# Kernel optimization log

Measured on AMD Instinct MI355X. Metric: run time of the kernel, lower is better.

Reference implementation:

```python
import jax, jax.numpy as jnp
import numpy as np

B, S, E = 2, 2048, 2048
H, KV, HD = 16, 4, 128  # num_heads, num_kv_heads, head_dim
G = H // KV             # query heads per kv head
ROPE_BASE = 10000.0


def rope_tables(dim, maxlen):
    freqs = 1.0 / ROPE_BASE ** (jnp.arange(0, dim, 2, dtype=jnp.float32) / dim)
    t = jnp.arange(maxlen, dtype=jnp.float32)
    f = jnp.outer(t, freqs)  # (maxlen, dim//2)
    return jnp.cos(f), jnp.sin(f)


def apply_rope(x, cos, sin):
    # x: (..., seq, heads, head_dim); interleaved-pair rotation
    s_len = x.shape[-3]
    c = cos[:s_len][:, None, :]
    s = sin[:s_len][:, None, :]
    x1 = x[..., ::2]
    x2 = x[..., 1::2]
    return jnp.stack([x1 * c - x2 * s, x1 * s + x2 * c], axis=-1).reshape(x.shape)


def setup_inputs() -> dict:
    key = jax.random.key(0)
    kx, kq, kk, kv, ko = jax.random.split(key, 5)
    x = jax.random.normal(kx, (B, S, E), dtype=jnp.float32)
    Wq = jax.random.normal(kq, (E, H * HD), dtype=jnp.float32) * 0.02
    Wk = jax.random.normal(kk, (E, KV * HD), dtype=jnp.float32) * 0.02
    Wv = jax.random.normal(kv, (E, KV * HD), dtype=jnp.float32) * 0.02
    Wo = jax.random.normal(ko, (H * HD, E), dtype=jnp.float32) * 0.02
    mask = jnp.tril(jnp.ones((S, S), dtype=bool))[None, None]  # causal (1,1,S,S)
    return {"x": x, "Wq": Wq, "Wk": Wk, "Wv": Wv, "Wo": Wo, "mask": mask}


def reference(x, Wq, Wk, Wv, Wo, mask):
    b, s, _ = x.shape
    cos, sin = rope_tables(HD, s)
    q = (x @ Wq).reshape(b, s, H, HD)
    k = (x @ Wk).reshape(b, s, KV, HD)
    v = (x @ Wv).reshape(b, s, KV, HD)
    q = apply_rope(q, cos, sin)
    k = apply_rope(k, cos, sin)
    if G > 1:
        k = jnp.repeat(k, G, axis=2)  # (b, s, H, HD)
        v = jnp.repeat(v, G, axis=2)
    q = jnp.transpose(q, (0, 2, 1, 3))  # (b, H, s, HD)
    k = jnp.transpose(k, (0, 2, 1, 3))
    v = jnp.transpose(v, (0, 2, 1, 3))
    scale = jnp.sqrt(jnp.float32(HD)).astype(q.dtype)
    scores = jnp.einsum("bhqd,bhkd->bhqk", q, k) / scale
    scores = jnp.where(mask, scores, jnp.finfo(scores.dtype).min)
    attn = jax.nn.softmax(scores, axis=-1)
    out = jnp.einsum("bhqk,bhkd->bhqd", attn, v)
    out = jnp.transpose(out, (0, 2, 1, 3)).reshape(b, s, H * HD)
    return out @ Wo
```

## Files before the change

### kernel.cpp

```cpp
#include <hip/hip_runtime.h>
#include <hip/hip_bf16.h>
#include <cstdint>

#define B_ 2
#define S_ 2048
#define E_ 2048
#define H_ 16
#define KV_ 4
#define HD_ 128
#define BS_ (B_*S_)
#define QKV_LD 3072
#define SM_SCALE 0.08838834764831845f
#define SC_LOG2E 0.1275424488538497f

typedef __attribute__((ext_vector_type(8))) __bf16 bf16x8;
typedef __attribute__((ext_vector_type(4))) float  floatx4;

__device__ __forceinline__ unsigned short f2bf(float f) {
  union { float f; unsigned u; } v; v.f = f;
  unsigned r = v.u + 0x7fffu + ((v.u >> 16) & 1u);
  return (unsigned short)(r >> 16);
}
__device__ __forceinline__ float bf2f(unsigned short u) {
  union { unsigned u; float f; } v; v.u = ((unsigned)u) << 16; return v.f;
}
__device__ __forceinline__ unsigned pack_bf16x2(float a, float b) {
  union { __hip_bfloat162 h; unsigned u; } v;
  v.h = __float22bfloat162_rn(make_float2(a, b));
  return v.u;
}

__device__ __forceinline__ void async_cp16(const void* g, void* l) {
  __builtin_amdgcn_global_load_lds(
      (const __attribute__((address_space(1))) void*)g,
      (__attribute__((address_space(3))) void*)l, 16, 0, 0);
}

__global__ __launch_bounds__(256)
void cvt_bf16(const float* __restrict__ src, unsigned short* __restrict__ dst,
              int n4) {
  int idx = blockIdx.x * 256 + threadIdx.x;
  if (idx >= n4) return;
  float4 v = *(const float4*)(src + (size_t)idx * 4);
  ushort4 o;
  o.x = f2bf(v.x); o.y = f2bf(v.y); o.z = f2bf(v.z); o.w = f2bf(v.w);
  *(ushort4*)(dst + (size_t)idx * 4) = o;
}

__global__ __launch_bounds__(256)
void cvt_bf16_t(const float* __restrict__ src, unsigned short* __restrict__ dst,
                int N, int dld, int noff) {
  __shared__ float tile[64 * 65];
  const int t = threadIdx.x;
  const int bk = blockIdx.y * 64, bn = blockIdx.x * 64;
  const int r = t >> 2, cg = t & 3;
#pragma unroll
  for (int i = 0; i < 4; ++i) {
    int c = cg * 16 + i * 4;
    float4 v = *(const float4*)(src + (size_t)(bk + r) * N + bn + c);
    tile[r * 65 + c] = v.x; tile[r * 65 + c + 1] = v.y;
    tile[r * 65 + c + 2] = v.z; tile[r * 65 + c + 3] = v.w;
  }
  __syncthreads();
  const int nl = t >> 2, kg = t & 3;
  union { unsigned short u[16]; uint4 q[2]; } o;
#pragma unroll
  for (int j = 0; j < 16; ++j)
    o.u[j] = f2bf(tile[(kg * 16 + j) * 65 + nl]);
  unsigned short* dp = dst + (size_t)(noff + bn + nl) * dld + bk + kg * 16;
  *(uint4*)(dp) = o.q[0];
  *(uint4*)(dp + 8) = o.q[1];
}

__global__ __launch_bounds__(256)
void rope_kernel(unsigned short* __restrict__ qkv) {
  const int PPR = 1280;
  int idx = blockIdx.x * 256 + threadIdx.x;
  if (idx >= BS_ * PPR) return;
  int row = idx / PPR, p = idx - row * PPR;
  int col = (p < 1024) ? (2 * p) : (2048 + 2 * (p - 1024));
  int d = p & 63;
  int s = row & (S_ - 1);
  float freq = expf(-(float)d * 0.14391156831212787f);
  float ang = (float)s * freq;
  float c = cosf(ang), sn = sinf(ang);
  unsigned short* ptr = qkv + (size_t)row * QKV_LD + col;
  float x1 = bf2f(ptr[0]), x2 = bf2f(ptr[1]);
  ptr[0] = f2bf(x1 * c - x2 * sn);
  ptr[1] = f2bf(x1 * sn + x2 * c);
}

__global__ __launch_bounds__(256)
void vtrans_kernel(const unsigned short* __restrict__ qkv,
                   unsigned short* __restrict__ vt) {
  __shared__ unsigned short tile[64 * 72];
  const int tid = threadIdx.x;
  const int s0 = blockIdx.x * 64;
  const int g = blockIdx.y >> 1;
  const int hh = (blockIdx.y & 1) * 64;
  const int b = g >> 2, kvh = g & 3;
#pragma unroll
  for (int i = 0; i < 2; ++i) {
    int chunk = tid + i * 256;
    int r = chunk >> 3, c = (chunk & 7) * 8;
    uint4 v = *(const uint4*)(qkv + (size_t)(b * S_ + s0 + r) * QKV_LD + 2560 + kvh * HD_ + hh + c);
    *(uint4*)(tile + r * 72 + c) = v;
  }
  __syncthreads();
#pragma unroll
  for (int i = 0; i < 2; ++i) {
    int chunk = tid + i * 256;
    int hdr = chunk >> 3, sc = (chunk & 7) * 8;
    union { unsigned short u[8]; uint4 v; } t;
#pragma unroll
    for (int j = 0; j < 8; ++j) t.u[j] = tile[(sc + j) * 72 + hdr];
    *(uint4*)(vt + (size_t)(g * HD_ + hh + hdr) * S_ + s0 + sc) = t.v;
  }
}

template<bool OUT_BF16>
__global__ __launch_bounds__(256, 2)
void gemm_tn(const unsigned short* __restrict__ A,
             const unsigned short* __restrict__ BT,
             void* __restrict__ C, int M, int N, int K) {
  __shared__ unsigned short Ash[128 * 32];
  __shared__ unsigned short Bsh[128 * 32];
  const int tid = threadIdx.x;
  const int l = tid & 63;
  const int l16 = l & 15, l4 = l >> 4;
  const int wave = tid >> 6;
  const int wm = (wave >> 1) * 64, wn = (wave & 1) * 64;
  const int bm = blockIdx.y * 128, bn = blockIdx.x * 128;

  const int srow = l >> 2;
  const int sg = (((l & 3) - (l >> 4)) & 3) * 8;

  floatx4 acc[4][4] = {};

  for (int kb = 0; kb < K; kb += 32) {
    __syncthreads();
#pragma unroll
    for (int i = 0; i < 2; ++i) {
      int cc = wave + i * 4;
      async_cp16(A + (size_t)(bm + 16 * cc + srow) * K + kb + sg, &Ash[cc * 512]);
      async_cp16(BT + (size_t)(bn + 16 * cc + srow) * K + kb + sg, &Bsh[cc * 512]);
    }
    __syncthreads();
    bf16x8 af[4], bf[4];
#pragma unroll
    for (int t = 0; t < 4; ++t) {
      int row = wm + t * 16 + l16;
      int s = (l4 + (l16 >> 2)) & 3;
      af[t] = *(const bf16x8*)(Ash + row * 32 + s * 8);
    }
#pragma unroll
    for (int t = 0; t < 4; ++t) {
      int row = wn + t * 16 + l16;
      int s = (l4 + (l16 >> 2)) & 3;
      bf[t] = *(const bf16x8*)(Bsh + row * 32 + s * 8);
    }
#pragma unroll
    for (int tm = 0; tm < 4; ++tm)
#pragma unroll
      for (int tn = 0; tn < 4; ++tn)
        acc[tm][tn] = __builtin_amdgcn_mfma_f32_16x16x32_bf16(af[tm], bf[tn], acc[tm][tn], 0, 0, 0);
  }
#pragma unroll
  for (int tm = 0; tm < 4; ++tm)
#pragma unroll
    for (int tn = 0; tn < 4; ++tn)
#pragma unroll
      for (int r = 0; r < 4; ++r) {
        int row = bm + wm + tm * 16 + l4 * 4 + r;
        int col = bn + wn + tn * 16 + l16;
        float v = acc[tm][tn][r];
        if (OUT_BF16) ((unsigned short*)C)[(size_t)row * N + col] = f2bf(v);
        else          ((float*)C)[(size_t)row * N + col] = v;
      }
}

__global__ __launch_bounds__(256, 2)
void gqa_attention(const unsigned short* __restrict__ qkv,
                   const unsigned short* __restrict__ vt,
                   unsigned short* __restrict__ out) {
  __shared__ unsigned short Ksh[2][32 * 128];
  __shared__ unsigned short Vsh[2][128 * 32];
  __shared__ unsigned short Psh[4][16 * 40];

  const int tid = threadIdx.x, l = tid & 63, wave = tid >> 6;
  const int l16 = l & 15, l4 = l >> 4;
  const int g = blockIdx.x, b = g >> 2, kvh = g & 3;
  const int h = kvh * 4 + wave;

  const int k_subrow = l >> 4;
  const int v_subrow = l >> 2;
  const int gv = (((l & 3) - (l >> 4)) & 3) * 8;

  for (int phase = 0; phase < 2; ++phase) {
    const int t = phase ? (127 - (int)blockIdx.y) : (int)blockIdx.y;
    const int qt = t * 16;
    const int nch = (qt >> 5) + 1;

    bf16x8 qf[4];
    {
      const unsigned short* qp = qkv + (size_t)(b * S_ + qt + l16) * QKV_LD + h * HD_;
#pragma unroll
      for (int c = 0; c < 4; ++c)
        qf[c] = *(const bf16x8*)(qp + c * 32 + l4 * 8);
    }
    asm volatile("s_waitcnt vmcnt(0)" ::: "memory");

#pragma unroll
    for (int i = 0; i < 2; ++i) {
      int cc = wave + i * 4;
      int krow = 4 * cc + k_subrow;
      int gk = (((l & 15) - krow) & 15) * 8;
      async_cp16(qkv + (size_t)(b * S_ + krow) * QKV_LD + 2048 + kvh * HD_ + gk,
                 &Ksh[0][cc * 512]);
      async_cp16(vt + (size_t)(g * HD_ + 16 * cc + v_subrow) * S_ + gv,
                 &Vsh[0][cc * 512]);
    }

    float lsum = 0.f;
    floatx4 acc[8] = {};

    for (int it = 0; it < nch; ++it) {
      const int kb = it * 32;
      const int cur = it & 1;
      asm volatile("s_barrier" ::: "memory");
      {
        const int kb2 = (it + 1 < nch) ? kb + 32 : 0;
#pragma unroll
        for (int i = 0; i < 2; ++i) {
          int cc = wave + i * 4;
          int krow = 4 * cc + k_subrow;
          int gk = (((l & 15) - krow) & 15) * 8;
          async_cp16(qkv + (size_t)(b * S_ + kb2 + krow) * QKV_LD + 2048 + kvh * HD_ + gk,
                     &Ksh[cur ^ 1][cc * 512]);
          async_cp16(vt + (size_t)(g * HD_ + 16 * cc + v_subrow) * S_ + kb2 + gv,
                     &Vsh[cur ^ 1][cc * 512]);
        }
      }
      asm volatile("s_waitcnt vmcnt(4)\n\ts_barrier" ::: "memory");

      floatx4 sacc[2] = {};
#pragma unroll
      for (int half = 0; half < 2; ++half) {
        int krow = half * 16 + l16;
#pragma unroll
        for (int c = 0; c < 4; ++c) {
          int s = (c * 4 + l4 + l16) & 15;
          bf16x8 kf = *(const bf16x8*)(&Ksh[cur][krow * 128 + s * 8]);
          sacc[half] = __builtin_amdgcn_mfma_f32_16x16x32_bf16(kf, qf[c], sacc[half], 0, 0, 0);
        }
      }
      float p[8];
      const bool need_mask = (kb + 31 > qt);
#pragma unroll
      for (int half = 0; half < 2; ++half)
#pragma unroll
        for (int r = 0; r < 4; ++r) {
          float v = fminf(sacc[half][r] * SC_LOG2E, 80.f);
          if (need_mask) {
            int ka = kb + half * 16 + l4 * 4 + r;
            if (ka > qt + l16) v = -3e38f;
          }
          float e = exp2f(v);
          p[half * 4 + r] = e;
          lsum += e;
        }
#pragma unroll
      for (int half = 0; half < 2; ++half) {
        uint2 pk;
        pk.x = pack_bf16x2(p[half * 4 + 0], p[half * 4 + 1]);
        pk.y = pack_bf16x2(p[half * 4 + 2], p[half * 4 + 3]);
        *(uint2*)(&Psh[wave][l16 * 40 + half * 16 + l4 * 4]) = pk;
      }
      bf16x8 pf = *(const bf16x8*)(&Psh[wave][l16 * 40 + l4 * 8]);
#pragma unroll
      for (int u = 0; u < 8; ++u) {
        int row = u * 16 + l16;
        int s = (l4 + (l16 >> 2)) & 3;
        bf16x8 vf = *(const bf16x8*)(&Vsh[cur][row * 32 + s * 8]);
        acc[u] = __builtin_amdgcn_mfma_f32_16x16x32_bf16(vf, pf, acc[u], 0, 0, 0);
      }
    }
    asm volatile("s_barrier" ::: "memory");

    lsum += __shfl_xor(lsum, 16, 64);
    lsum += __shfl_xor(lsum, 32, 64);
    float inv = 1.0f / lsum;
    unsigned short* op = out + (size_t)(b * S_ + qt + l16) * 2048 + h * HD_;
#pragma unroll
    for (int u = 0; u < 8; ++u) {
      uint2 o;
      o.x = pack_bf16x2(acc[u][0] * inv, acc[u][1] * inv);
      o.y = pack_bf16x2(acc[u][2] * inv, acc[u][3] * inv);
      *(uint2*)(op + u * 16 + l4 * 4) = o;
    }
  }
}

extern "C" void kernel_launch(void* const* d_in, const int* in_sizes, int n_in,
                              void* d_out, int out_size, void* d_ws, size_t ws_size,
                              hipStream_t stream) {
  const float* x  = (const float*)d_in[0];
  const float* Wq = (const float*)d_in[1];
  const float* Wk = (const float*)d_in[2];
  const float* Wv = (const float*)d_in[3];
  const float* Wo = (const float*)d_in[4];
  float* out = (float*)d_out;

  char* ws = (char*)d_ws;
  unsigned short* xb    = (unsigned short*)(ws);
  unsigned short* wqkvT = (unsigned short*)(ws + 16777216);
  unsigned short* woT   = (unsigned short*)(ws + 29360128);
  unsigned short* qkv   = (unsigned short*)(ws + 37748736);
  unsigned short* attn  = (unsigned short*)(ws + 62914560);
  unsigned short* vt    = (unsigned short*)(ws);

  cvt_bf16<<<(4096 * 2048 / 4 + 255) / 256, 256, 0, stream>>>(x, xb, 4096 * 2048 / 4);
  cvt_bf16_t<<<dim3(32, 32), 256, 0, stream>>>(Wq, wqkvT, 2048, 2048, 0);
  cvt_bf16_t<<<dim3(8, 32),  256, 0, stream>>>(Wk, wqkvT, 512,  2048, 2048);
  cvt_bf16_t<<<dim3(8, 32),  256, 0, stream>>>(Wv, wqkvT, 512,  2048, 2560);
  cvt_bf16_t<<<dim3(32, 32), 256, 0, stream>>>(Wo, woT,  2048, 2048, 0);

  gemm_tn<true><<<dim3(24, 32), 256, 0, stream>>>(xb, wqkvT, qkv, 4096, 3072, 2048);
  rope_kernel<<<(4096 * 1280 + 255) / 256, 256, 0, stream>>>(qkv);
  vtrans_kernel<<<dim3(32, 16), 256, 0, stream>>>(qkv, vt);
  gqa_attention<<<dim3(8, 64), 256, 0, stream>>>(qkv, vt, attn);
  gemm_tn<false><<<dim3(16, 32), 256, 0, stream>>>(attn, woT, out, 4096, 2048, 2048);
}
```

Before: 337.6 us.

## Drop LDS P staging via permlane swaps, one q-tile per block, raise occupancy

The attention kernel now launches one block per 16-row query tile, heaviest tiles first, instead of pairing two tiles per block. It also rearranges the softmax probabilities into the MFMA operand layout with permlane32/16 swaps rather than a round-trip through LDS, and it raises the launch-bounds occupancy hint from 2 to 4. K/V pointer math is hoisted out of the loop and the MFMA sections get raised wave priority. The aim is less LDS traffic and more waves in flight to hide latency, at the cost of tighter register budgets (possible spills) and less explicit load balancing across blocks.

```diff
diff --git a/kernel.cpp b/kernel.cpp
--- a/kernel.cpp
+++ b/kernel.cpp
@@ -179,13 +179,12 @@
       }
 }
 
-__global__ __launch_bounds__(256, 2)
+__global__ __launch_bounds__(256, 4)
 void gqa_attention(const unsigned short* __restrict__ qkv,
                    const unsigned short* __restrict__ vt,
                    unsigned short* __restrict__ out) {
   __shared__ unsigned short Ksh[2][32 * 128];
   __shared__ unsigned short Vsh[2][128 * 32];
-  __shared__ unsigned short Psh[4][16 * 40];
 
   const int tid = threadIdx.x, l = tid & 63, wave = tid >> 6;
   const int l16 = l & 15, l4 = l >> 4;
@@ -196,108 +195,119 @@
   const int v_subrow = l >> 2;
   const int gv = (((l & 3) - (l >> 4)) & 3) * 8;
 
-  for (int phase = 0; phase < 2; ++phase) {
-    const int t = phase ? (127 - (int)blockIdx.y) : (int)blockIdx.y;
-    const int qt = t * 16;
-    const int nch = (qt >> 5) + 1;
-
-    bf16x8 qf[4];
+  const int t = 127 - (int)blockIdx.y;
+  const int qt = t * 16;
+  const int nch = (qt >> 5) + 1;
+
+  bf16x8 qf[4];
+  {
+    const unsigned short* qp = qkv + (size_t)(b * S_ + qt + l16) * QKV_LD + h * HD_;
+#pragma unroll
+    for (int c = 0; c < 4; ++c)
+      qf[c] = *(const bf16x8*)(qp + c * 32 + l4 * 8);
+  }
+  asm volatile("s_waitcnt vmcnt(0)" ::: "memory");
+
+  const unsigned short* kp[2];
+  const unsigned short* vp[2];
+#pragma unroll
+  for (int i = 0; i < 2; ++i) {
+    int cc = wave + i * 4;
+    int krow = 4 * cc + k_subrow;
+    int gk = (((l & 15) - krow) & 15) * 8;
+    kp[i] = qkv + (size_t)(b * S_ + krow) * QKV_LD + 2048 + kvh * HD_ + gk;
+    vp[i] = vt + (size_t)(g * HD_ + 16 * cc + v_subrow) * S_ + gv;
+  }
+
+#pragma unroll
+  for (int i = 0; i < 2; ++i) {
+    int cc = wave + i * 4;
+    async_cp16(kp[i], &Ksh[0][cc * 512]);
+    async_cp16(vp[i], &Vsh[0][cc * 512]);
+  }
+
+  float lsum = 0.f;
+  floatx4 acc[8] = {};
+
+  for (int it = 0; it < nch; ++it) {
+    const int kb = it * 32;
+    const int cur = it & 1;
+    asm volatile("s_barrier" ::: "memory");
     {
-      const unsigned short* qp = qkv + (size_t)(b * S_ + qt + l16) * QKV_LD + h * HD_;
-#pragma unroll
-      for (int c = 0; c < 4; ++c)
-        qf[c] = *(const bf16x8*)(qp + c * 32 + l4 * 8);
-    }
-    asm volatile("s_waitcnt vmcnt(0)" ::: "memory");
-
-#pragma unroll
-    for (int i = 0; i < 2; ++i) {
-      int cc = wave + i * 4;
-      int krow = 4 * cc + k_subrow;
-      int gk = (((l & 15) - krow) & 15) * 8;
-      async_cp16(qkv + (size_t)(b * S_ + krow) * QKV_LD + 2048 + kvh * HD_ + gk,
-                 &Ksh[0][cc * 512]);
-      async_cp16(vt + (size_t)(g * HD_ + 16 * cc + v_subrow) * S_ + gv,
-                 &Vsh[0][cc * 512]);
-    }
-
-    float lsum = 0.f;
-    floatx4 acc[8] = {};
-
-    for (int it = 0; it < nch; ++it) {
-      const int kb = it * 32;
-      const int cur = it & 1;
-      asm volatile("s_barrier" ::: "memory");
-      {
-        const int kb2 = (it + 1 < nch) ? kb + 32 : 0;
-#pragma unroll
-        for (int i = 0; i < 2; ++i) {
-          int cc = wave + i * 4;
-          int krow = 4 * cc + k_subrow;
-          int gk = (((l & 15) - krow) & 15) * 8;
-          async_cp16(qkv + (size_t)(b * S_ + kb2 + krow) * QKV_LD + 2048 + kvh * HD_ + gk,
-                     &Ksh[cur ^ 1][cc * 512]);
-          async_cp16(vt + (size_t)(g * HD_ + 16 * cc + v_subrow) * S_ + kb2 + gv,
-                     &Vsh[cur ^ 1][cc * 512]);
+      const int kb2 = (it + 1 < nch) ? kb + 32 : 0;
+      const int ko = kb2 * QKV_LD;
+#pragma unroll
+      for (int i = 0; i < 2; ++i) {
+        int cc = wave + i * 4;
+        async_cp16(kp[i] + ko, &Ksh[cur ^ 1][cc * 512]);
+        async_cp16(vp[i] + kb2, &Vsh[cur ^ 1][cc * 512]);
+      }
+    }
+    asm volatile("s_waitcnt vmcnt(4)\n\ts_barrier" ::: "memory");
+
+    floatx4 sacc[2] = {};
+    __builtin_amdgcn_s_setprio(1);
+#pragma unroll
+    for (int half = 0; half < 2; ++half) {
+      int krow = half * 16 + l16;
+#pragma unroll
+      for (int c = 0; c < 4; ++c) {
+        int s = (c * 4 + l4 + l16) & 15;
+        bf16x8 kf = *(const bf16x8*)(&Ksh[cur][krow * 128 + s * 8]);
+        sacc[half] = __builtin_amdgcn_mfma_f32_16x16x32_bf16(kf, qf[c], sacc[half], 0, 0, 0);
+      }
+    }
+    __builtin_amdgcn_s_setprio(0);
+
+    float p[8];
+    const bool need_mask = (kb + 31 > qt);
+#pragma unroll
+    for (int half = 0; half < 2; ++half)
+#pragma unroll
+      for (int r = 0; r < 4; ++r) {
+        float v = fminf(sacc[half][r] * SC_LOG2E, 80.f);
+        if (need_mask) {
+          int ka = kb + half * 16 + l4 * 4 + r;
+          if (ka > qt + l16) v = -3e38f;
         }
+        float e = exp2f(v);
+        p[half * 4 + r] = e;
+        lsum += e;
       }
-      asm volatile("s_waitcnt vmcnt(4)\n\ts_barrier" ::: "memory");
-
-      floatx4 sacc[2] = {};
-#pragma unroll
-      for (int half = 0; half < 2; ++half) {
-        int krow = half * 16 + l16;
-#pragma unroll
-        for (int c = 0; c < 4; ++c) {
-          int s = (c * 4 + l4 + l16) & 15;
-          bf16x8 kf = *(const bf16x8*)(&Ksh[cur][krow * 128 + s * 8]);
-          sacc[half] = __builtin_amdgcn_mfma_f32_16x16x32_bf16(kf, qf[c], sacc[half], 0, 0, 0);
-        }
-      }
-      float p[8];
-      const bool need_mask = (kb + 31 > qt);
-#pragma unroll
-      for (int half = 0; half < 2; ++half)
-#pragma unroll
-        for (int r = 0; r < 4; ++r) {
-          float v = fminf(sacc[half][r] * SC_LOG2E, 80.f);
-          if (need_mask) {
-            int ka = kb + half * 16 + l4 * 4 + r;
-            if (ka > qt + l16) v = -3e38f;
-          }
-          float e = exp2f(v);
-          p[half * 4 + r] = e;
-          lsum += e;
-        }
-#pragma unroll
-      for (int half = 0; half < 2; ++half) {
-        uint2 pk;
-        pk.x = pack_bf16x2(p[half * 4 + 0], p[half * 4 + 1]);
-        pk.y = pack_bf16x2(p[half * 4 + 2], p[half * 4 + 3]);
-        *(uint2*)(&Psh[wave][l16 * 40 + half * 16 + l4 * 4]) = pk;
-      }
-      bf16x8 pf = *(const bf16x8*)(&Psh[wave][l16 * 40 + l4 * 8]);
-#pragma unroll
-      for (int u = 0; u < 8; ++u) {
-        int row = u * 16 + l16;
-        int s = (l4 + (l16 >> 2)) & 3;
-        bf16x8 vf = *(const bf16x8*)(&Vsh[cur][row * 32 + s * 8]);
-        acc[u] = __builtin_amdgcn_mfma_f32_16x16x32_bf16(vf, pf, acc[u], 0, 0, 0);
-      }
-    }
-    asm volatile("s_barrier" ::: "memory");
-
-    lsum += __shfl_xor(lsum, 16, 64);
-    lsum += __shfl_xor(lsum, 32, 64);
-    float inv = 1.0f / lsum;
-    unsigned short* op = out + (size_t)(b * S_ + qt + l16) * 2048 + h * HD_;
+
+    unsigned u0 = pack_bf16x2(p[0], p[1]);
+    unsigned u1 = pack_bf16x2(p[2], p[3]);
+    unsigned u2 = pack_bf16x2(p[4], p[5]);
+    unsigned u3 = pack_bf16x2(p[6], p[7]);
+    asm("v_permlane32_swap_b32 %0, %1" : "+v"(u0), "+v"(u2));
+    asm("v_permlane16_swap_b32 %0, %1" : "+v"(u0), "+v"(u2));
+    asm("v_permlane32_swap_b32 %0, %1" : "+v"(u1), "+v"(u3));
+    asm("v_permlane16_swap_b32 %0, %1" : "+v"(u1), "+v"(u3));
+    union { unsigned w[4]; bf16x8 v8; } pun;
+    pun.w[0] = u0; pun.w[1] = u1; pun.w[2] = u2; pun.w[3] = u3;
+    const bf16x8 pf = pun.v8;
+
+    __builtin_amdgcn_s_setprio(1);
 #pragma unroll
     for (int u = 0; u < 8; ++u) {
-      uint2 o;
-      o.x = pack_bf16x2(acc[u][0] * inv, acc[u][1] * inv);
-      o.y = pack_bf16x2(acc[u][2] * inv, acc[u][3] * inv);
-      *(uint2*)(op + u * 16 + l4 * 4) = o;
-    }
+      int row = u * 16 + l16;
+      int s = (l4 + (l16 >> 2)) & 3;
+      bf16x8 vf = *(const bf16x8*)(&Vsh[cur][row * 32 + s * 8]);
+      acc[u] = __builtin_amdgcn_mfma_f32_16x16x32_bf16(vf, pf, acc[u], 0, 0, 0);
+    }
+    __builtin_amdgcn_s_setprio(0);
+  }
+
+  lsum += __shfl_xor(lsum, 16, 64);
+  lsum += __shfl_xor(lsum, 32, 64);
+  float inv = 1.0f / lsum;
+  unsigned short* op = out + (size_t)(b * S_ + qt + l16) * 2048 + h * HD_;
+#pragma unroll
+  for (int u = 0; u < 8; ++u) {
+    uint2 o;
+    o.x = pack_bf16x2(acc[u][0] * inv, acc[u][1] * inv);
+    o.y = pack_bf16x2(acc[u][2] * inv, acc[u][3] * inv);
+    *(uint2*)(op + u * 16 + l4 * 4) = o;
   }
 }
 
@@ -328,6 +338,6 @@
   gemm_tn<true><<<dim3(24, 32), 256, 0, stream>>>(xb, wqkvT, qkv, 4096, 3072, 2048);
   rope_kernel<<<(4096 * 1280 + 255) / 256, 256, 0, stream>>>(qkv);
   vtrans_kernel<<<dim3(32, 16), 256, 0, stream>>>(qkv, vt);
-  gqa_attention<<<dim3(8, 64), 256, 0, stream>>>(qkv, vt, attn);
+  gqa_attention<<<dim3(8, 128), 256, 0, stream>>>(qkv, vt, attn);
   gemm_tn<false><<<dim3(16, 32), 256, 0, stream>>>(attn, woT, out, 4096, 2048, 2048);
 }
```

New measurement: 338.9 us. Within noise of the previous version (+0.4%).
